# Kernel tuning notes

Hardware: AMD Instinct MI355X
Metric: run time of the kernel (lower is better)

The kernel has to match this reference:

```python
import jax, jax.numpy as jnp
import numpy as np

H = 4096
DFF = 16384
EPS = 1e-5

def _layernorm(x, gamma, beta, eps):
    mu = jnp.mean(x, axis=-1, keepdims=True)
    var = jnp.var(x, axis=-1, keepdims=True)
    return (x - mu) * jax.lax.rsqrt(var + eps) * gamma + beta

def setup_inputs() -> dict:
    key = jax.random.key(0)
    ks = jax.random.split(key, 9)
    B, S = 2, 2048
    s_h = 1.0 / np.sqrt(H)
    s_f = 1.0 / np.sqrt(DFF)
    return {
        "input": jax.random.normal(ks[0], (B, S, H), jnp.float32),
        "residual": jax.random.normal(ks[1], (B, S, H), jnp.float32),
        "residual_norm": jax.random.normal(ks[2], (B, S, H), jnp.float32),
        "bias": jax.random.normal(ks[3], (H,), jnp.float32) * 0.02,
        "attn_nw": 1.0 + jax.random.normal(ks[4], (H,), jnp.float32) * 0.02,
        "attn_nb": jax.random.normal(ks[5], (H,), jnp.float32) * 0.02,
        "inter_w": jax.random.normal(ks[6], (H, DFF), jnp.float32) * s_h,
        "inter_b": jax.random.normal(ks[7], (DFF,), jnp.float32) * 0.02,
        "output_w": jax.random.normal(ks[8], (DFF, H), jnp.float32) * s_f,
        "output_b": jnp.zeros((H,), jnp.float32),
    }

def reference(input, residual, residual_norm, bias, attn_nw, attn_nb,
              inter_w, inter_b, output_w, output_b):
    # mlp_gemm (pre_layer_norm, mlp_after_attn, fp32, no quant):
    # LN(input + residual + attn_bias) -> GEMM -> GeLU -> GEMM
    ln_in = input + residual + bias                      # [B,S,H]
    ln = _layernorm(ln_in, attn_nw, attn_nb, EPS)        # [B,S,H]
    inter = jax.nn.gelu(jnp.einsum('bsh,hf->bsf', ln, inter_w) + inter_b,
                        approximate=True)                # [B,S,DFF]
    out = jnp.einsum('bsf,fh->bsh', inter, output_w)     # [B,S,H]
    # residual_add (preln, add_bias, mp_size=1):
    # residual = mlp_out + residual + attn_out + (attn_bias + mlp_bias)/mp_size
    return out + residual + input + (bias + output_b)
```

## Files before the change

### kernel.cpp

```cpp
#include <hip/hip_runtime.h>
#include <cstdint>
#include <cstddef>

#define H_DIM 4096
#define DFF_DIM 16384
#define NROWS 4096

typedef unsigned short bf16_t;
typedef __attribute__((ext_vector_type(8))) short bf16x8;
typedef __attribute__((ext_vector_type(4))) float f32x4;
typedef __attribute__((ext_vector_type(4))) unsigned short u16x4;

static __device__ __forceinline__ bf16_t f2bf(float f) {
  union { float f; unsigned int i; } v; v.f = f;
  unsigned int x = v.i;
  return (bf16_t)((x + 0x7fffu + ((x >> 16) & 1u)) >> 16);
}

#define GLDS16(gp, lp)                                                    \
  __builtin_amdgcn_global_load_lds(                                       \
      (__attribute__((address_space(1))) void*)(gp),                      \
      (__attribute__((address_space(3))) void*)(lp), 16, 0, 0)

__global__ __launch_bounds__(256) void fused_ln_kernel(
    const float* __restrict__ inp, const float* __restrict__ res,
    const float* __restrict__ bias, const float* __restrict__ gamma,
    const float* __restrict__ beta, bf16_t* __restrict__ out) {
  int row = blockIdx.x;
  int t = threadIdx.x;
  const float4* pin = (const float4*)(inp + (size_t)row * H_DIM);
  const float4* pre = (const float4*)(res + (size_t)row * H_DIM);
  const float4* pbi = (const float4*)bias;
  float4 xv[4];
  float s = 0.f, ss = 0.f;
#pragma unroll
  for (int i = 0; i < 4; ++i) {
    int idx = t + i * 256;
    float4 a = pin[idx];
    float4 b = pre[idx];
    float4 c = pbi[idx];
    float4 v;
    v.x = a.x + b.x + c.x;
    v.y = a.y + b.y + c.y;
    v.z = a.z + b.z + c.z;
    v.w = a.w + b.w + c.w;
    xv[i] = v;
    s += v.x + v.y + v.z + v.w;
    ss += v.x * v.x + v.y * v.y + v.z * v.z + v.w * v.w;
  }
#pragma unroll
  for (int off = 32; off > 0; off >>= 1) {
    s += __shfl_xor(s, off);
    ss += __shfl_xor(ss, off);
  }
  __shared__ float sred[8];
  int w = t >> 6, l = t & 63;
  if (l == 0) { sred[w] = s; sred[4 + w] = ss; }
  __syncthreads();
  s = sred[0] + sred[1] + sred[2] + sred[3];
  ss = sred[4] + sred[5] + sred[6] + sred[7];
  const float inv = 1.f / (float)H_DIM;
  float mean = s * inv;
  float var = ss * inv - mean * mean;
  float rstd = rsqrtf(var + 1e-5f);
  const float4* pg = (const float4*)gamma;
  const float4* pb = (const float4*)beta;
#pragma unroll
  for (int i = 0; i < 4; ++i) {
    int idx = t + i * 256;
    float4 g = pg[idx];
    float4 bb = pb[idx];
    float4 v = xv[i];
    u16x4 o;
    o.x = f2bf((v.x - mean) * rstd * g.x + bb.x);
    o.y = f2bf((v.y - mean) * rstd * g.y + bb.y);
    o.z = f2bf((v.z - mean) * rstd * g.z + bb.z);
    o.w = f2bf((v.w - mean) * rstd * g.w + bb.w);
    *(u16x4*)(out + (size_t)row * H_DIM + (size_t)idx * 4) = o;
  }
}

__global__ __launch_bounds__(256) void transpose_cvt_kernel(
    const float* __restrict__ W, bf16_t* __restrict__ Wt, int K, int N) {
  __shared__ float tile[64][65];
  int nb = N >> 6;
  int bk = blockIdx.x / nb;
  int bn = blockIdx.x - bk * nb;
  int t = threadIdx.x;
  int r = t >> 4;
  int c4 = (t & 15) << 2;
#pragma unroll
  for (int p = 0; p < 4; ++p) {
    int row = r + p * 16;
    float4 v = *(const float4*)(W + (size_t)(bk * 64 + row) * N + bn * 64 + c4);
    tile[row][c4 + 0] = v.x;
    tile[row][c4 + 1] = v.y;
    tile[row][c4 + 2] = v.z;
    tile[row][c4 + 3] = v.w;
  }
  __syncthreads();
#pragma unroll
  for (int p = 0; p < 4; ++p) {
    int nn = r + p * 16;
    u16x4 o;
    o.x = f2bf(tile[c4 + 0][nn]);
    o.y = f2bf(tile[c4 + 1][nn]);
    o.z = f2bf(tile[c4 + 2][nn]);
    o.w = f2bf(tile[c4 + 3][nn]);
    *(u16x4*)(Wt + (size_t)(bn * 64 + nn) * K + bk * 64 + c4) = o;
  }
}

#define QMFMA(AQ, BQ, MILO, NJLO)                                           \
  __builtin_amdgcn_s_setprio(1);                                            \
  _Pragma("unroll") for (int k5 = 0; k5 < 2; ++k5)                          \
  _Pragma("unroll") for (int i5 = 0; i5 < 4; ++i5)                          \
  _Pragma("unroll") for (int j5 = 0; j5 < 2; ++j5)                          \
    acc[MILO + i5][NJLO + j5] = __builtin_amdgcn_mfma_f32_16x16x32_bf16(    \
        AQ[i5 * 2 + k5], BQ[j5 * 2 + k5], acc[MILO + i5][NJLO + j5], 0, 0, 0); \
  __builtin_amdgcn_s_setprio(0);

#define BAR __builtin_amdgcn_s_barrier()
#define LGKM0 asm volatile("s_waitcnt lgkmcnt(0)" ::: "memory")
#define LGKM8 asm volatile("s_waitcnt lgkmcnt(8)" ::: "memory")
#define VM6 asm volatile("s_waitcnt vmcnt(6)" ::: "memory")

template <int EPI>
__global__ __launch_bounds__(512, 2) void gemm8p_kernel(
    const bf16_t* __restrict__ A, const bf16_t* __restrict__ Bt,
    int M, int N, int K,
    const float* __restrict__ eb1, const float* __restrict__ eb2,
    const float* __restrict__ add1, const float* __restrict__ add2,
    bf16_t* __restrict__ outb, float* __restrict__ outf) {
  __shared__ char lds[131072];

  const int t = threadIdx.x;
  const int l = t & 63;
  const int wid = t >> 6;
  const int wr = wid >> 2;
  const int wc = wid & 3;

  int nwg = gridDim.x;
  int bid = blockIdx.x;
  int wg = (bid & 7) * (nwg >> 3) + (bid >> 3);
  int ntm = M >> 8;
  int chunk = wg >> 5, s5 = wg & 31;
  int cmn = ntm >> 3;
  int cm = chunk % cmn, cn = chunk / cmn;
  int tm = cm * 8 + (s5 & 7);
  int tn = cn * 4 + (s5 >> 3);
  size_t m0 = (size_t)tm * 256, n0 = (size_t)tn * 256;

  f32x4 acc[8][4];
#pragma unroll
  for (int i = 0; i < 8; ++i)
#pragma unroll
    for (int j = 0; j < 4; ++j) acc[i][j] = {0.f, 0.f, 0.f, 0.f};

  const int rh = t >> 3;
  const int sl = t & 7;
  const int oc = sl ^ ((rh >> 1) & 7);
  const bf16_t* sA0 = A + (m0 + rh) * (size_t)K + oc * 8;
  const bf16_t* sA1 = A + (m0 + rh + 64) * (size_t)K + oc * 8;
  const bf16_t* sB0 = Bt + (n0 + rh) * (size_t)K + oc * 8;
  const bf16_t* sB1 = Bt + (n0 + rh + 64) * (size_t)K + oc * 8;

  auto stA = [&](int b, int h, int T) {
    GLDS16(sA0 + (size_t)h * 128 * K + (size_t)T * 64,
           lds + b * 32768 + h * 16384 + t * 16);
    GLDS16(sA1 + (size_t)h * 128 * K + (size_t)T * 64,
           lds + b * 32768 + h * 16384 + (t + 512) * 16);
  };
  auto stB = [&](int b, int h, int T) {
    GLDS16(sB0 + (size_t)h * 128 * K + (size_t)T * 64,
           lds + 65536 + b * 32768 + h * 16384 + t * 16);
    GLDS16(sB1 + (size_t)h * 128 * K + (size_t)T * 64,
           lds + 65536 + b * 32768 + h * 16384 + (t + 512) * 16);
  };

  int offA[8][2], offB[4][2];
#pragma unroll
  for (int mi = 0; mi < 8; ++mi) {
    int h = mi >> 2;
    int lr = (mi & 3) * 32 + wr * 16 + (l & 15);
#pragma unroll
    for (int ks = 0; ks < 2; ++ks) {
      int o = ks * 4 + (l >> 4);
      offA[mi][ks] = h * 16384 + lr * 128 + ((o ^ ((lr >> 1) & 7)) << 4);
    }
  }
#pragma unroll
  for (int nj = 0; nj < 4; ++nj) {
    int h = nj >> 1;
    int lc = (nj & 1) * 64 + wc * 16 + (l & 15);
#pragma unroll
    for (int ks = 0; ks < 2; ++ks) {
      int o = ks * 4 + (l >> 4);
      offB[nj][ks] = 65536 + h * 16384 + lc * 128 + ((o ^ ((lc >> 1) & 7)) << 4);
    }
  }

  auto rd8 = [&](int off) -> bf16x8 {
    return *(const bf16x8*)(const void*)(lds + off);
  };

  const int NT = K >> 6;
  const int NI = NT >> 1;

  stB(0, 0, 0); stA(0, 0, 0); stB(0, 1, 0); stA(0, 1, 0);
  stB(1, 0, 1); stA(1, 0, 1); stB(1, 1, 1);
  VM6;
  BAR;

  bf16x8 aQ[8], bQ0[4], bQ1[4];
  for (int it = 0; it < NI; ++it) {
    const int Tb = 2 * it + 1;
    int Sa = 2 * it + 2; if (Sa >= NT) Sa = NT - 1;
    int Sb = 2 * it + 3; if (Sb >= NT) Sb = NT - 1;

#pragma unroll
    for (int i = 0; i < 4; ++i)
#pragma unroll
      for (int ks = 0; ks < 2; ++ks) aQ[i * 2 + ks] = rd8(offA[i][ks]);
#pragma unroll
    for (int j = 0; j < 2; ++j)
#pragma unroll
      for (int ks = 0; ks < 2; ++ks) bQ0[j * 2 + ks] = rd8(offB[j][ks]);
    stA(1, 1, Tb);
    LGKM8; BAR; LGKM0;
    QMFMA(aQ, bQ0, 0, 0)
    BAR;
#pragma unroll
    for (int j = 0; j < 2; ++j)
#pragma unroll
      for (int ks = 0; ks < 2; ++ks) bQ1[j * 2 + ks] = rd8(offB[2 + j][ks]);
    stB(0, 0, Sa);
    BAR; LGKM0;
    QMFMA(aQ, bQ1, 0, 2)
    BAR;
#pragma unroll
    for (int i = 0; i < 4; ++i)
#pragma unroll
      for (int ks = 0; ks < 2; ++ks) aQ[i * 2 + ks] = rd8(offA[4 + i][ks]);
    stA(0, 0, Sa);
    BAR; LGKM0;
    QMFMA(aQ, bQ1, 4, 2)
    BAR;
    stB(0, 1, Sa);
    VM6; BAR;
    QMFMA(aQ, bQ0, 4, 0)
    BAR;

#pragma unroll
    for (int i = 0; i < 4; ++i)
#pragma unroll
      for (int ks = 0; ks < 2; ++ks) aQ[i * 2 + ks] = rd8(32768 + offA[i][ks]);
#pragma unroll
    for (int j = 0; j < 2; ++j)
#pragma unroll
      for (int ks = 0; ks < 2; ++ks) bQ0[j * 2 + ks] = rd8(32768 + offB[j][ks]);
    stA(0, 1, Sa);
    LGKM8; BAR; LGKM0;
    QMFMA(aQ, bQ0, 0, 0)
    BAR;
#pragma unroll
    for (int j = 0; j < 2; ++j)
#pragma unroll
      for (int ks = 0; ks < 2; ++ks)
        bQ1[j * 2 + ks] = rd8(32768 + offB[2 + j][ks]);
    stB(1, 0, Sb);
    BAR; LGKM0;
    QMFMA(aQ, bQ1, 0, 2)
    BAR;
#pragma unroll
    for (int i = 0; i < 4; ++i)
#pragma unroll
      for (int ks = 0; ks < 2; ++ks)
        aQ[i * 2 + ks] = rd8(32768 + offA[4 + i][ks]);
    stA(1, 0, Sb);
    BAR; LGKM0;
    QMFMA(aQ, bQ1, 4, 2)
    BAR;
    stB(1, 1, Sb);
    VM6; BAR;
    QMFMA(aQ, bQ0, 4, 0)
    BAR;
  }
  asm volatile("s_waitcnt vmcnt(0)" ::: "memory");

  int lr4 = (l >> 4) * 4;
  int lc = l & 15;
#pragma unroll
  for (int mi = 0; mi < 8; ++mi) {
#pragma unroll
    for (int i2 = 0; i2 < 4; ++i2) {
      int rrow = (int)m0 + (mi * 2 + wr) * 16 + lr4 + i2;
      size_t base = (size_t)rrow * N;
#pragma unroll
      for (int nj = 0; nj < 4; ++nj) {
        int col = (int)n0 + (nj * 4 + wc) * 16 + lc;
        float v = acc[mi][nj][i2];
        if (EPI == 0) {
          float x = v + eb1[col];
          float u = 0.7978845608028654f * (x + 0.044715f * x * x * x);
          float th = 1.f - 2.f / (__expf(2.f * u) + 1.f);
          outb[base + col] = f2bf(0.5f * x * (1.f + th));
        } else {
          outf[base + col] =
              v + eb1[col] + eb2[col] + add1[base + col] + add2[base + col];
        }
      }
    }
  }
}

extern "C" void kernel_launch(void* const* d_in, const int* in_sizes, int n_in,
                              void* d_out, int out_size, void* d_ws,
                              size_t ws_size, hipStream_t stream) {
  const float* input = (const float*)d_in[0];
  const float* residual = (const float*)d_in[1];
  const float* bias = (const float*)d_in[3];
  const float* attn_nw = (const float*)d_in[4];
  const float* attn_nb = (const float*)d_in[5];
  const float* inter_w = (const float*)d_in[6];
  const float* inter_b = (const float*)d_in[7];
  const float* output_w = (const float*)d_in[8];
  const float* output_b = (const float*)d_in[9];
  float* out = (float*)d_out;

  char* ws = (char*)d_ws;
  bf16_t* lnb = (bf16_t*)ws;
  bf16_t* w1t = (bf16_t*)(ws + (size_t)NROWS * H_DIM * 2);
  bf16_t* w2t = (bf16_t*)(ws + (size_t)NROWS * H_DIM * 2 +
                          (size_t)H_DIM * DFF_DIM * 2);
  bf16_t* inter = (bf16_t*)(ws + (size_t)NROWS * H_DIM * 2 +
                            2 * (size_t)H_DIM * DFF_DIM * 2);

  fused_ln_kernel<<<NROWS, 256, 0, stream>>>(input, residual, bias, attn_nw,
                                             attn_nb, lnb);
  transpose_cvt_kernel<<<(H_DIM / 64) * (DFF_DIM / 64), 256, 0, stream>>>(
      inter_w, w1t, H_DIM, DFF_DIM);
  transpose_cvt_kernel<<<(DFF_DIM / 64) * (H_DIM / 64), 256, 0, stream>>>(
      output_w, w2t, DFF_DIM, H_DIM);
  gemm8p_kernel<0><<<(NROWS / 256) * (DFF_DIM / 256), 512, 0, stream>>>(
      lnb, w1t, NROWS, DFF_DIM, H_DIM, inter_b, nullptr, nullptr, nullptr,
      inter, nullptr);
  gemm8p_kernel<1><<<(NROWS / 256) * (H_DIM / 256), 512, 0, stream>>>(
      inter, w2t, NROWS, H_DIM, DFF_DIM, bias, output_b, residual, input,
      nullptr, out);
}
```

Measured before the change: 1.076 ms.

## Interleave LDS fragment reads with MFMA halves to software-pipeline the GEMM loop

The per-quadrant MFMA block is split into two k-halves, and the LDS reads for the next quadrant's fragments are issued between them instead of before a full lgkmcnt(0) wait. The first fragment loads are hoisted before the loop, and each iteration's tail prefetches the next iteration's fragments. This is meant to hide LDS read latency behind matrix math and remove the explicit lgkmcnt waits. The risk is that the explicit waits are gone and the code now depends on the compiler inserting correct waits. Register reuse around the barriers, where fragments are overwritten while other waves store, could also be a hazard.

```diff
diff --git a/kernel.cpp b/kernel.cpp
--- a/kernel.cpp
+++ b/kernel.cpp
@@ -111,18 +111,15 @@
   }
 }
 
-#define QMFMA(AQ, BQ, MILO, NJLO)                                           \
+#define QMFMA_H(AQ, BQ, MILO, NJLO, K5)                                     \
   __builtin_amdgcn_s_setprio(1);                                            \
-  _Pragma("unroll") for (int k5 = 0; k5 < 2; ++k5)                          \
   _Pragma("unroll") for (int i5 = 0; i5 < 4; ++i5)                          \
   _Pragma("unroll") for (int j5 = 0; j5 < 2; ++j5)                          \
     acc[MILO + i5][NJLO + j5] = __builtin_amdgcn_mfma_f32_16x16x32_bf16(    \
-        AQ[i5 * 2 + k5], BQ[j5 * 2 + k5], acc[MILO + i5][NJLO + j5], 0, 0, 0); \
+        AQ[i5 * 2 + K5], BQ[j5 * 2 + K5], acc[MILO + i5][NJLO + j5], 0, 0, 0); \
   __builtin_amdgcn_s_setprio(0);
 
 #define BAR __builtin_amdgcn_s_barrier()
-#define LGKM0 asm volatile("s_waitcnt lgkmcnt(0)" ::: "memory")
-#define LGKM8 asm volatile("s_waitcnt lgkmcnt(8)" ::: "memory")
 #define VM6 asm volatile("s_waitcnt vmcnt(6)" ::: "memory")
 
 template <int EPI>
@@ -213,77 +210,86 @@
   BAR;
 
   bf16x8 aQ[8], bQ0[4], bQ1[4];
+#pragma unroll
+  for (int i = 0; i < 4; ++i)
+#pragma unroll
+    for (int ks = 0; ks < 2; ++ks) aQ[i * 2 + ks] = rd8(offA[i][ks]);
+#pragma unroll
+  for (int j = 0; j < 2; ++j)
+#pragma unroll
+    for (int ks = 0; ks < 2; ++ks) bQ0[j * 2 + ks] = rd8(offB[j][ks]);
+
   for (int it = 0; it < NI; ++it) {
     const int Tb = 2 * it + 1;
     int Sa = 2 * it + 2; if (Sa >= NT) Sa = NT - 1;
     int Sb = 2 * it + 3; if (Sb >= NT) Sb = NT - 1;
 
-#pragma unroll
-    for (int i = 0; i < 4; ++i)
-#pragma unroll
-      for (int ks = 0; ks < 2; ++ks) aQ[i * 2 + ks] = rd8(offA[i][ks]);
-#pragma unroll
-    for (int j = 0; j < 2; ++j)
-#pragma unroll
-      for (int ks = 0; ks < 2; ++ks) bQ0[j * 2 + ks] = rd8(offB[j][ks]);
     stA(1, 1, Tb);
-    LGKM8; BAR; LGKM0;
-    QMFMA(aQ, bQ0, 0, 0)
-    BAR;
-#pragma unroll
-    for (int j = 0; j < 2; ++j)
-#pragma unroll
-      for (int ks = 0; ks < 2; ++ks) bQ1[j * 2 + ks] = rd8(offB[2 + j][ks]);
+    BAR;
+    QMFMA_H(aQ, bQ0, 0, 0, 0)
+    bQ1[0] = rd8(offB[2][0]); bQ1[2] = rd8(offB[3][0]);
+    QMFMA_H(aQ, bQ0, 0, 0, 1)
+    bQ1[1] = rd8(offB[2][1]); bQ1[3] = rd8(offB[3][1]);
+    BAR;
     stB(0, 0, Sa);
-    BAR; LGKM0;
-    QMFMA(aQ, bQ1, 0, 2)
-    BAR;
-#pragma unroll
-    for (int i = 0; i < 4; ++i)
-#pragma unroll
-      for (int ks = 0; ks < 2; ++ks) aQ[i * 2 + ks] = rd8(offA[4 + i][ks]);
+    BAR;
+    QMFMA_H(aQ, bQ1, 0, 2, 0)
+    aQ[0] = rd8(offA[4][0]); aQ[2] = rd8(offA[5][0]);
+    aQ[4] = rd8(offA[6][0]); aQ[6] = rd8(offA[7][0]);
+    QMFMA_H(aQ, bQ1, 0, 2, 1)
+    aQ[1] = rd8(offA[4][1]); aQ[3] = rd8(offA[5][1]);
+    aQ[5] = rd8(offA[6][1]); aQ[7] = rd8(offA[7][1]);
+    BAR;
     stA(0, 0, Sa);
-    BAR; LGKM0;
-    QMFMA(aQ, bQ1, 4, 2)
+    BAR;
+    QMFMA_H(aQ, bQ1, 4, 2, 0)
+    QMFMA_H(aQ, bQ1, 4, 2, 1)
     BAR;
     stB(0, 1, Sa);
-    VM6; BAR;
-    QMFMA(aQ, bQ0, 4, 0)
-    BAR;
-
-#pragma unroll
-    for (int i = 0; i < 4; ++i)
-#pragma unroll
-      for (int ks = 0; ks < 2; ++ks) aQ[i * 2 + ks] = rd8(32768 + offA[i][ks]);
-#pragma unroll
-    for (int j = 0; j < 2; ++j)
-#pragma unroll
-      for (int ks = 0; ks < 2; ++ks) bQ0[j * 2 + ks] = rd8(32768 + offB[j][ks]);
+    VM6;
+    BAR;
+    QMFMA_H(aQ, bQ0, 4, 0, 0)
+    bQ0[0] = rd8(32768 + offB[0][0]); bQ0[2] = rd8(32768 + offB[1][0]);
+    aQ[0] = rd8(32768 + offA[0][0]); aQ[2] = rd8(32768 + offA[1][0]);
+    aQ[4] = rd8(32768 + offA[2][0]); aQ[6] = rd8(32768 + offA[3][0]);
+    QMFMA_H(aQ, bQ0, 4, 0, 1)
+    bQ0[1] = rd8(32768 + offB[0][1]); bQ0[3] = rd8(32768 + offB[1][1]);
+    aQ[1] = rd8(32768 + offA[0][1]); aQ[3] = rd8(32768 + offA[1][1]);
+    aQ[5] = rd8(32768 + offA[2][1]); aQ[7] = rd8(32768 + offA[3][1]);
+    BAR;
+
     stA(0, 1, Sa);
-    LGKM8; BAR; LGKM0;
-    QMFMA(aQ, bQ0, 0, 0)
-    BAR;
-#pragma unroll
-    for (int j = 0; j < 2; ++j)
-#pragma unroll
-      for (int ks = 0; ks < 2; ++ks)
-        bQ1[j * 2 + ks] = rd8(32768 + offB[2 + j][ks]);
+    BAR;
+    QMFMA_H(aQ, bQ0, 0, 0, 0)
+    bQ1[0] = rd8(32768 + offB[2][0]); bQ1[2] = rd8(32768 + offB[3][0]);
+    QMFMA_H(aQ, bQ0, 0, 0, 1)
+    bQ1[1] = rd8(32768 + offB[2][1]); bQ1[3] = rd8(32768 + offB[3][1]);
+    BAR;
     stB(1, 0, Sb);
-    BAR; LGKM0;
-    QMFMA(aQ, bQ1, 0, 2)
-    BAR;
-#pragma unroll
-    for (int i = 0; i < 4; ++i)
-#pragma unroll
-      for (int ks = 0; ks < 2; ++ks)
-        aQ[i * 2 + ks] = rd8(32768 + offA[4 + i][ks]);
+    BAR;
+    QMFMA_H(aQ, bQ1, 0, 2, 0)
+    aQ[0] = rd8(32768 + offA[4][0]); aQ[2] = rd8(32768 + offA[5][0]);
+    aQ[4] = rd8(32768 + offA[6][0]); aQ[6] = rd8(32768 + offA[7][0]);
+    QMFMA_H(aQ, bQ1, 0, 2, 1)
+    aQ[1] = rd8(32768 + offA[4][1]); aQ[3] = rd8(32768 + offA[5][1]);
+    aQ[5] = rd8(32768 + offA[6][1]); aQ[7] = rd8(32768 + offA[7][1]);
+    BAR;
     stA(1, 0, Sb);
-    BAR; LGKM0;
-    QMFMA(aQ, bQ1, 4, 2)
+    BAR;
+    QMFMA_H(aQ, bQ1, 4, 2, 0)
+    QMFMA_H(aQ, bQ1, 4, 2, 1)
     BAR;
     stB(1, 1, Sb);
-    VM6; BAR;
-    QMFMA(aQ, bQ0, 4, 0)
+    VM6;
+    BAR;
+    QMFMA_H(aQ, bQ0, 4, 0, 0)
+    bQ0[0] = rd8(offB[0][0]); bQ0[2] = rd8(offB[1][0]);
+    aQ[0] = rd8(offA[0][0]); aQ[2] = rd8(offA[1][0]);
+    aQ[4] = rd8(offA[2][0]); aQ[6] = rd8(offA[3][0]);
+    QMFMA_H(aQ, bQ0, 4, 0, 1)
+    bQ0[1] = rd8(offB[0][1]); bQ0[3] = rd8(offB[1][1]);
+    aQ[1] = rd8(offA[0][1]); aQ[3] = rd8(offA[1][1]);
+    aQ[5] = rd8(offA[2][1]); aQ[7] = rd8(offA[3][1]);
     BAR;
   }
   asm volatile("s_waitcnt vmcnt(0)" ::: "memory");
```

New measurement: 1.065 ms. No clear change (-1.0%).
